# Kernel tuning notes

Hardware: AMD Instinct MI355X
Metric: run time of the kernel (lower is better)

The kernel has to match this reference:

```python
import jax, jax.numpy as jnp
import numpy as np


def fwht(x):
    """Fast Walsh-Hadamard transform over the last dim (power of 2), normalized by 1/sqrt(n)."""
    n = x.shape[-1]
    orig_shape = x.shape
    x = x.reshape(-1, n)
    h = 1
    while h < n:
        x = x.reshape(-1, n // (2 * h), 2, h)
        a = x[:, :, 0, :]
        b = x[:, :, 1, :]
        x = jnp.stack([a + b, a - b], axis=2)
        h *= 2
    x = x.reshape(orig_shape)
    return x * (1.0 / jnp.sqrt(jnp.asarray(n, dtype=x.dtype)))


def act_quant(x, bits):
    """Per-token absmax symmetric quantization with straight-through estimator."""
    qb = 2.0 ** (bits - 1) - 1.0  # 127 for 8 bits
    scale = qb / jnp.clip(jnp.max(jnp.abs(x), axis=-1, keepdims=True), 1e-5, None)
    q = jnp.clip(jnp.round(x * scale), -qb, qb) / scale
    return x + jax.lax.stop_gradient(q - x)


def weight_quant(w):
    """BitNet b1.58 ternary weight quantization (per-tensor mean-abs scale) with STE."""
    scale = jnp.clip(jnp.mean(jnp.abs(w)), 1e-5, None)
    q = jnp.clip(jnp.round(w / scale), -1.0, 1.0) * scale
    return w + jax.lax.stop_gradient(q - w)


def hbitlinear(x, w, bits):
    # Hadamard rotate activations, quantize acts + ternary weights, then GEMM.
    xh = fwht(x)
    xq = act_quant(xh, bits)
    wq = weight_quant(w)
    return jnp.einsum('bsh,oh->bso', xq, wq)


def setup_inputs() -> dict:
    key = jax.random.key(0)
    k1, k2, k3 = jax.random.split(key, 3)
    B, S, H = 4, 2048, 2048
    I = 4096  # intermediate = hidden * mlp_ratio(2.0)
    hidden_states = jax.random.normal(k1, (B, S, H), dtype=jnp.float32)
    w_up = jax.random.normal(k2, (I, H), dtype=jnp.float32) * 0.02
    w_down = jax.random.normal(k3, (H, I), dtype=jnp.float32) * 0.02
    return {"hidden_states": hidden_states, "w_up": w_up, "w_down": w_down}


def reference(hidden_states, w_up, w_down):
    ACT_BITS = 8
    h = hbitlinear(hidden_states, w_up, ACT_BITS)   # (B, S, I)
    h = jnp.square(jax.nn.relu(h))                  # ReLU^2
    # dropout with p=0.0 (eval/identity)
    out = hbitlinear(h, w_down, ACT_BITS)           # (B, S, H)
    return out
```

## Files before the change

### kernel.cpp

```cpp
#include <hip/hip_runtime.h>
#include <hip/hip_bf16.h>
#include <hip/hip_fp16.h>

typedef int i32x4 __attribute__((ext_vector_type(4)));

#define GLL16(g, l) __builtin_amdgcn_global_load_lds( \
    (const __attribute__((address_space(1))) void*)(g), \
    (__attribute__((address_space(3))) void*)(l), 16, 0, 0)

#define CFENCE() asm volatile("" ::: "memory")

__global__ __launch_bounds__(256) void abs_sum2_kernel(const float* __restrict__ w0,
                                                       const float* __restrict__ w1, int n4,
                                                       double* __restrict__ out)
{
    const int sel = blockIdx.x & 1;
    const float4* w4 = (const float4*)(sel ? w1 : w0);
    const int b = blockIdx.x >> 1, nb = gridDim.x >> 1;
    double acc = 0.0;
    for (int i = b * blockDim.x + threadIdx.x; i < n4; i += nb * blockDim.x) {
        float4 v = w4[i];
        acc += (double)fabsf(v.x) + (double)fabsf(v.y) + (double)fabsf(v.z) + (double)fabsf(v.w);
    }
    for (int o = 32; o > 0; o >>= 1) acc += __shfl_down(acc, o, 64);
    __shared__ double part[4];
    int lane = threadIdx.x & 63, wv = threadIdx.x >> 6;
    if (lane == 0) part[wv] = acc;
    __syncthreads();
    if (threadIdx.x == 0) atomicAdd(&out[sel], part[0] + part[1] + part[2] + part[3]);
}

__global__ __launch_bounds__(256) void wquant2_kernel(const float* __restrict__ w0,
                                                      const float* __restrict__ w1, int n4,
                                                      const double* __restrict__ sums, double inv_count,
                                                      char* __restrict__ o0, char* __restrict__ o1)
{
    const int sel = blockIdx.x & 1;
    const float4* w4 = (const float4*)(sel ? w1 : w0);
    char4* o4 = (char4*)(sel ? o1 : o0);
    float s = (float)(sums[sel] * inv_count);
    s = fmaxf(s, 1e-5f);
    const int b = blockIdx.x >> 1, nb = gridDim.x >> 1;
    for (int i = b * blockDim.x + threadIdx.x; i < n4; i += nb * blockDim.x) {
        float4 v = w4[i];
        char4 c;
        c.x = (char)fminf(fmaxf(rintf(v.x / s), -1.0f), 1.0f);
        c.y = (char)fminf(fmaxf(rintf(v.y / s), -1.0f), 1.0f);
        c.z = (char)fminf(fmaxf(rintf(v.z / s), -1.0f), 1.0f);
        c.w = (char)fminf(fmaxf(rintf(v.w / s), -1.0f), 1.0f);
        o4[i] = c;
    }
}

template<int NS>
__device__ __forceinline__ void hreg(float* v)
{
    #pragma unroll
    for (int h = 1; h < (1 << NS); h <<= 1)
        #pragma unroll
        for (int i = 0; i < 16; i++)
            if ((i & h) == 0) { float a = v[i], b = v[i + h]; v[i] = a + b; v[i + h] = a - b; }
}

__device__ __forceinline__ int lswz(int e)
{
    const int r16 = e >> 4;
    return r16 * 16 + 4 * (((e >> 2) & 3) ^ ((r16 >> 1) & 3)) + (e & 3);
}

template<int N, int TOKS>
__global__ __launch_bounds__(256) void fwht_quant_kernel(
    const float* __restrict__ in, long in_stride,
    char* __restrict__ outq, long out_stride,
    float* __restrict__ scales)
{
    constexpr int L = 256 / TOKS;
    static_assert(N == 16 * L, "N must be 16*threads-per-token");
    __shared__ float sx[TOKS * N];
    __shared__ float red[4];

    const int tid = threadIdx.x;
    const int tk  = tid / L;
    const int lt  = tid % L;
    const long tok = (long)blockIdx.x * TOKS + tk;
    const float* row = in + tok * in_stride;
    float* s = sx + tk * N;

    float v[16];
    {
        const float4* r4 = (const float4*)(row + (size_t)lt * 16);
        float4 a[4];
        #pragma unroll
        for (int i = 0; i < 4; i++) a[i] = r4[i];
        #pragma unroll
        for (int i = 0; i < 4; i++) {
            v[4*i] = a[i].x; v[4*i+1] = a[i].y; v[4*i+2] = a[i].z; v[4*i+3] = a[i].w;
        }
    }
    hreg<4>(v);
    {
        const int psw = (lt >> 1) & 3;
        #pragma unroll
        for (int i = 0; i < 4; i++)
            *(float4*)(s + lt * 16 + 4 * (i ^ psw)) =
                make_float4(v[4*i], v[4*i+1], v[4*i+2], v[4*i+3]);
    }
    __syncthreads();

    const int o = lt & 15, ss = lt >> 4;
    #pragma unroll
    for (int j = 0; j < 16; j++) v[j] = s[lswz(o + 256 * ss + 16 * j)];
    hreg<(L == 256) ? 4 : 3>(v);
    #pragma unroll
    for (int j = 0; j < 16; j++) s[lswz(o + 256 * ss + 16 * j)] = v[j];
    __syncthreads();

    #pragma unroll
    for (int j = 0; j < 16; j++) v[j] = s[lswz(o + 16 * ss + L * j)];
    hreg<4>(v);

    const float rn = 1.0f / sqrtf((float)N);
    float m = 0.0f;
    #pragma unroll
    for (int j = 0; j < 16; j++) { v[j] *= rn; m = fmaxf(m, fabsf(v[j])); }
    for (int off = 32; off > 0; off >>= 1) m = fmaxf(m, __shfl_down(m, off, 64));
    if ((tid & 63) == 0) red[tid >> 6] = m;
    __syncthreads();
    float mm;
    if (TOKS == 1) mm = fmaxf(fmaxf(red[0], red[1]), fmaxf(red[2], red[3]));
    else           mm = fmaxf(red[2 * tk], red[2 * tk + 1]);
    mm = fmaxf(mm, 1e-5f);
    const float sc = 127.0f / mm;
    if (lt == 0) scales[tok] = sc;
    __syncthreads();

    char* ct = (char*)sx + tk * N;
    #pragma unroll
    for (int j = 0; j < 16; j++) {
        float q = fminf(fmaxf(rintf(v[j] * sc), -127.0f), 127.0f);
        ct[o + 16 * ss + L * j] = (char)q;
    }
    __syncthreads();
    int4* dst = (int4*)(outq + tok * out_stride);
    dst[lt] = ((const int4*)ct)[lt];
}

__global__ __launch_bounds__(256) void fwht_quant_f16_kernel(
    const __half* __restrict__ in, long in_stride,
    char* __restrict__ outq, long out_stride,
    float* __restrict__ scales)
{
    constexpr int N = 4096, L = 256;
    __shared__ float sx[N];
    __shared__ float red[4];

    const int lt = threadIdx.x;
    const long tok = blockIdx.x;
    const __half* row = in + tok * in_stride;
    float* s = sx;

    float v[16];
    {
        const int4* r4 = (const int4*)row;
        int4 q0 = r4[2 * lt], q1 = r4[2 * lt + 1];
        const __half2* h0 = (const __half2*)&q0;
        const __half2* h1 = (const __half2*)&q1;
        #pragma unroll
        for (int i = 0; i < 4; i++) {
            float2 f = __half22float2(h0[i]);
            v[2*i] = f.x; v[2*i+1] = f.y;
        }
        #pragma unroll
        for (int i = 0; i < 4; i++) {
            float2 f = __half22float2(h1[i]);
            v[8+2*i] = f.x; v[8+2*i+1] = f.y;
        }
    }
    hreg<4>(v);
    {
        const int psw = (lt >> 1) & 3;
        #pragma unroll
        for (int i = 0; i < 4; i++)
            *(float4*)(s + lt * 16 + 4 * (i ^ psw)) =
                make_float4(v[4*i], v[4*i+1], v[4*i+2], v[4*i+3]);
    }
    __syncthreads();

    const int o = lt & 15, ss = lt >> 4;
    #pragma unroll
    for (int j = 0; j < 16; j++) v[j] = s[lswz(o + 256 * ss + 16 * j)];
    hreg<4>(v);
    #pragma unroll
    for (int j = 0; j < 16; j++) s[lswz(o + 256 * ss + 16 * j)] = v[j];
    __syncthreads();

    #pragma unroll
    for (int j = 0; j < 16; j++) v[j] = s[lswz(o + 16 * ss + L * j)];
    hreg<4>(v);

    const float rn = 1.0f / sqrtf((float)N);
    float m = 0.0f;
    #pragma unroll
    for (int j = 0; j < 16; j++) { v[j] *= rn; m = fmaxf(m, fabsf(v[j])); }
    for (int off = 32; off > 0; off >>= 1) m = fmaxf(m, __shfl_down(m, off, 64));
    if ((lt & 63) == 0) red[lt >> 6] = m;
    __syncthreads();
    float mm = fmaxf(fmaxf(red[0], red[1]), fmaxf(red[2], red[3]));
    mm = fmaxf(mm, 1e-5f);
    const float sc = 127.0f / mm;
    if (lt == 0) scales[tok] = sc;
    __syncthreads();

    char* ct = (char*)sx;
    #pragma unroll
    for (int j = 0; j < 16; j++) {
        float q = fminf(fmaxf(rintf(v[j] * sc), -127.0f), 127.0f);
        ct[o + 16 * ss + L * j] = (char)q;
    }
    __syncthreads();
    int4* dst = (int4*)(outq + tok * out_stride);
    dst[lt] = ((const int4*)ct)[lt];
}

#define BM2 256
#define BN2 256
#define BK2 64

__global__ __launch_bounds__(512, 2) void gemm_bt_kernel(
    const char* __restrict__ A, int lda,
    const char* __restrict__ B, int ldb,
    void* __restrict__ Cv, int ldc,
    int K, int lognx,
    const float* __restrict__ sx,
    const double* __restrict__ wsum, double inv_count,
    int do_relu2, int out_f16)
{
    __shared__ __align__(16) char As[4][BM2 * BK2];
    __shared__ __align__(16) char Bs[4][BN2 * BK2];

    const int bid = blockIdx.x;
    const int xcd = bid & 7;
    const int n = bid >> 3;
    const int nper = gridDim.x >> 3;
    const int bx = n & ((1 << lognx) - 1);
    const int by = xcd * (nper >> lognx) + (n >> lognx);
    const int row0 = by * BM2;
    const int col0 = bx * BN2;

    const int tid = threadIdx.x;
    const int lane = tid & 63;
    const int w = tid >> 6;
    const int wr = w >> 2;
    const int wc = w & 3;

    i32x4 acc[8][4] = {};

    const int srow = w * 16 + (lane >> 2);
    const int sseg = ((lane & 3) ^ ((lane >> 3) & 3)) << 4;
    const char* Ag0 = A + (size_t)(row0 + srow) * lda + sseg;
    const char* Ag1 = Ag0 + (size_t)128 * lda;
    const char* Bg0 = B + (size_t)(col0 + srow) * ldb + sseg;
    const char* Bg1 = Bg0 + (size_t)128 * ldb;
    const int wdst = w * 1024;

    const int fr = lane & 15;
    const int fks = lane >> 4;
    const int rsw = ((fks ^ ((fr >> 1) & 3)) << 4);
    const int aoff = (wr * 128 + fr) * BK2 + rsw;
    const int boff = (wc * 64  + fr) * BK2 + rsw;

    const int NT = K >> 6;

    auto stageA = [&](int tt) {
        const int sb = tt & 3;
        const int ko = tt * BK2;
        GLL16(Ag0 + ko, &As[sb][wdst]);
        GLL16(Ag1 + ko, &As[sb][wdst + 8192]);
    };
    auto stageB = [&](int tt) {
        const int sb = tt & 3;
        const int ko = tt * BK2;
        GLL16(Bg0 + ko, &Bs[sb][wdst]);
        GLL16(Bg1 + ko, &Bs[sb][wdst + 8192]);
    };

    auto tile_body = [&](int t, bool do_stage) __attribute__((always_inline)) {
        const int cb = t & 3;
        const char* as = As[cb];
        const char* bs = Bs[cb];
        i32x4 af[4], bf[4], af2[4];
        #pragma unroll
        for (int i = 0; i < 4; ++i) af[i] = *(const i32x4*)(as + aoff + i * 1024);
        #pragma unroll
        for (int j = 0; j < 4; ++j) bf[j] = *(const i32x4*)(bs + boff + j * 1024);
        if (do_stage) stageA(t + 3);
        __builtin_amdgcn_s_barrier();
        CFENCE();
        __builtin_amdgcn_s_setprio(1);
        #pragma unroll
        for (int i = 0; i < 4; ++i)
            #pragma unroll
            for (int j = 0; j < 4; ++j)
                acc[i][j] = __builtin_amdgcn_mfma_i32_16x16x64_i8(af[i], bf[j], acc[i][j], 0, 0, 0);
        __builtin_amdgcn_s_setprio(0);
        __builtin_amdgcn_s_barrier();
        CFENCE();
        #pragma unroll
        for (int i = 0; i < 4; ++i) af2[i] = *(const i32x4*)(as + aoff + (4 + i) * 1024);
        if (do_stage) stageB(t + 3);
        __builtin_amdgcn_s_barrier();
        CFENCE();
        __builtin_amdgcn_s_setprio(1);
        #pragma unroll
        for (int i = 0; i < 4; ++i)
            #pragma unroll
            for (int j = 0; j < 4; ++j)
                acc[4 + i][j] = __builtin_amdgcn_mfma_i32_16x16x64_i8(af2[i], bf[j], acc[4 + i][j], 0, 0, 0);
        __builtin_amdgcn_s_setprio(0);
    };

    stageA(0); stageB(0); stageA(1); stageB(1); stageA(2); stageB(2);
    asm volatile("s_waitcnt vmcnt(8)" ::: "memory");
    __builtin_amdgcn_s_barrier();
    CFENCE();

    for (int t = 0; t <= NT - 4; ++t) {
        tile_body(t, true);
        asm volatile("s_waitcnt vmcnt(8)" ::: "memory");
        __builtin_amdgcn_s_barrier();
        CFENCE();
    }
    tile_body(NT - 3, false);
    asm volatile("s_waitcnt vmcnt(4)" ::: "memory");
    __builtin_amdgcn_s_barrier();
    CFENCE();
    tile_body(NT - 2, false);
    asm volatile("s_waitcnt vmcnt(0)" ::: "memory");
    __builtin_amdgcn_s_barrier();
    CFENCE();
    tile_body(NT - 1, false);

    float sw = (float)(wsum[0] * inv_count);
    sw = fmaxf(sw, 1e-5f);
    const int qd = lane >> 4;
    if (out_f16) {
        __half* C = (__half*)Cv;
        #pragma unroll
        for (int i = 0; i < 8; ++i) {
            #pragma unroll
            for (int r = 0; r < 4; ++r) {
                int rowm = row0 + wr * 128 + i * 16 + qd * 4 + r;
                float esc = sw / sx[rowm];
                __half* crow = C + (size_t)rowm * ldc + col0 + wc * 64;
                #pragma unroll
                for (int j = 0; j < 4; ++j) {
                    float v = (float)acc[i][j][r] * esc;
                    if (do_relu2) { v = fmaxf(v, 0.0f); v = v * v; }
                    crow[j * 16 + fr] = __float2half(v);
                }
            }
        }
    } else {
        float* C = (float*)Cv;
        #pragma unroll
        for (int i = 0; i < 8; ++i) {
            #pragma unroll
            for (int r = 0; r < 4; ++r) {
                int rowm = row0 + wr * 128 + i * 16 + qd * 4 + r;
                float esc = sw / sx[rowm];
                float* crow = C + (size_t)rowm * ldc + col0 + wc * 64;
                #pragma unroll
                for (int j = 0; j < 4; ++j) {
                    float v = (float)acc[i][j][r] * esc;
                    if (do_relu2) { v = fmaxf(v, 0.0f); v = v * v; }
                    crow[j * 16 + fr] = v;
                }
            }
        }
    }
}

extern "C" void kernel_launch(void* const* d_in, const int* in_sizes, int n_in,
                              void* d_out, int out_size, void* d_ws, size_t ws_size,
                              hipStream_t stream)
{
    const float* X   = (const float*)d_in[0];
    const float* Wup = (const float*)d_in[1];
    const float* Wdn = (const float*)d_in[2];
    float* out = (float*)d_out;

    const int Mtok = 8192, H = 2048, I = 4096;
    const int NW = H * I;

    char* ws = (char*)d_ws;
    double* sums = (double*)ws;
    float* sx1 = (float*)(ws + 1024);
    float* sx2 = (float*)(ws + 1024 + 32768);
    char* wqup = ws + (1 << 20);
    char* wqdn = wqup + (size_t)NW;
    char* xq1  = wqdn + (size_t)NW;
    char* hbuf = xq1 + (size_t)Mtok * H;

    hipMemsetAsync(sums, 0, 16, stream);
    abs_sum2_kernel<<<1024, 256, 0, stream>>>(Wup, Wdn, NW / 4, sums);
    const double invc = 1.0 / (double)NW;
    wquant2_kernel<<<2048, 256, 0, stream>>>(Wup, Wdn, NW / 4, sums, invc, wqup, wqdn);

    fwht_quant_kernel<2048, 2><<<Mtok / 2, 256, 0, stream>>>(X, H, xq1, H, sx1);
    gemm_bt_kernel<<<(I / BN2) * (Mtok / BM2), 512, 0, stream>>>(
        xq1, H, wqup, H, hbuf, I, H, 4, sx1, &sums[0], invc, 1, 1);
    fwht_quant_f16_kernel<<<Mtok, 256, 0, stream>>>((const __half*)hbuf, I, hbuf, 2 * I, sx2);
    gemm_bt_kernel<<<(H / BN2) * (Mtok / BM2), 512, 0, stream>>>(
        (const char*)hbuf, 2 * I, wqdn, I, out, H, I, 3, sx2, &sums[1], invc, 0, 0);
}
```

Measured before the change: 372.3 us.

## Shrink GEMM tiles to 128x128 with simple double buffering; threshold weight ternarization

The int8 MFMA GEMM goes from 256x256 tiles with 512 threads and a 4-stage, split A/B prefetch pipeline to 128x128 tiles with 256 threads and a plain 2-stage double buffer that waits on all loads every iteration. Smaller tiles raise the block count and allow three blocks per CU, at the cost of less data reuse per tile and less overlap between loads and MFMA work. Weight quantization replaces the divide, round and clamp with a comparison against half the scale. That comparison can differ from the reference at exact ties.

```diff
diff --git a/kernel.cpp b/kernel.cpp
--- a/kernel.cpp
+++ b/kernel.cpp
@@ -40,14 +40,15 @@
     char4* o4 = (char4*)(sel ? o1 : o0);
     float s = (float)(sums[sel] * inv_count);
     s = fmaxf(s, 1e-5f);
+    const float t0 = 0.5f * s;
     const int b = blockIdx.x >> 1, nb = gridDim.x >> 1;
     for (int i = b * blockDim.x + threadIdx.x; i < n4; i += nb * blockDim.x) {
         float4 v = w4[i];
         char4 c;
-        c.x = (char)fminf(fmaxf(rintf(v.x / s), -1.0f), 1.0f);
-        c.y = (char)fminf(fmaxf(rintf(v.y / s), -1.0f), 1.0f);
-        c.z = (char)fminf(fmaxf(rintf(v.z / s), -1.0f), 1.0f);
-        c.w = (char)fminf(fmaxf(rintf(v.w / s), -1.0f), 1.0f);
+        c.x = (fabsf(v.x) > t0) ? (v.x > 0.0f ? 1 : -1) : 0;
+        c.y = (fabsf(v.y) > t0) ? (v.y > 0.0f ? 1 : -1) : 0;
+        c.z = (fabsf(v.z) > t0) ? (v.z > 0.0f ? 1 : -1) : 0;
+        c.w = (fabsf(v.w) > t0) ? (v.w > 0.0f ? 1 : -1) : 0;
         o4[i] = c;
     }
 }
@@ -222,11 +223,11 @@
     dst[lt] = ((const int4*)ct)[lt];
 }
 
-#define BM2 256
-#define BN2 256
-#define BK2 64
-
-__global__ __launch_bounds__(512, 2) void gemm_bt_kernel(
+#define BM 128
+#define BN 128
+#define BK 64
+
+__global__ __launch_bounds__(256, 3) void gemm_bt_kernel(
     const char* __restrict__ A, int lda,
     const char* __restrict__ B, int ldb,
     void* __restrict__ Cv, int ldc,
@@ -235,8 +236,8 @@
     const double* __restrict__ wsum, double inv_count,
     int do_relu2, int out_f16)
 {
-    __shared__ __align__(16) char As[4][BM2 * BK2];
-    __shared__ __align__(16) char Bs[4][BN2 * BK2];
+    __shared__ __align__(16) char As[2][BM * BK];
+    __shared__ __align__(16) char Bs[2][BN * BK];
 
     const int bid = blockIdx.x;
     const int xcd = bid & 7;
@@ -244,58 +245,49 @@
     const int nper = gridDim.x >> 3;
     const int bx = n & ((1 << lognx) - 1);
     const int by = xcd * (nper >> lognx) + (n >> lognx);
-    const int row0 = by * BM2;
-    const int col0 = bx * BN2;
+    const int row0 = by * BM;
+    const int col0 = bx * BN;
 
     const int tid = threadIdx.x;
     const int lane = tid & 63;
     const int w = tid >> 6;
-    const int wr = w >> 2;
-    const int wc = w & 3;
-
-    i32x4 acc[8][4] = {};
+    const int wr = w >> 1;
+    const int wc = w & 1;
+
+    i32x4 acc[4][4] = {};
 
     const int srow = w * 16 + (lane >> 2);
     const int sseg = ((lane & 3) ^ ((lane >> 3) & 3)) << 4;
     const char* Ag0 = A + (size_t)(row0 + srow) * lda + sseg;
-    const char* Ag1 = Ag0 + (size_t)128 * lda;
+    const char* Ag1 = Ag0 + (size_t)64 * lda;
     const char* Bg0 = B + (size_t)(col0 + srow) * ldb + sseg;
-    const char* Bg1 = Bg0 + (size_t)128 * ldb;
+    const char* Bg1 = Bg0 + (size_t)64 * ldb;
     const int wdst = w * 1024;
 
     const int fr = lane & 15;
     const int fks = lane >> 4;
     const int rsw = ((fks ^ ((fr >> 1) & 3)) << 4);
-    const int aoff = (wr * 128 + fr) * BK2 + rsw;
-    const int boff = (wc * 64  + fr) * BK2 + rsw;
+    const int aoff = (wr * 64 + fr) * BK + rsw;
+    const int boff = (wc * 64 + fr) * BK + rsw;
 
     const int NT = K >> 6;
 
-    auto stageA = [&](int tt) {
-        const int sb = tt & 3;
-        const int ko = tt * BK2;
+    auto stage = [&](int tt) {
+        const int sb = tt & 1;
+        const int ko = tt * BK;
         GLL16(Ag0 + ko, &As[sb][wdst]);
-        GLL16(Ag1 + ko, &As[sb][wdst + 8192]);
+        GLL16(Ag1 + ko, &As[sb][wdst + 4096]);
+        GLL16(Bg0 + ko, &Bs[sb][wdst]);
+        GLL16(Bg1 + ko, &Bs[sb][wdst + 4096]);
     };
-    auto stageB = [&](int tt) {
-        const int sb = tt & 3;
-        const int ko = tt * BK2;
-        GLL16(Bg0 + ko, &Bs[sb][wdst]);
-        GLL16(Bg1 + ko, &Bs[sb][wdst + 8192]);
-    };
-
-    auto tile_body = [&](int t, bool do_stage) __attribute__((always_inline)) {
-        const int cb = t & 3;
-        const char* as = As[cb];
-        const char* bs = Bs[cb];
-        i32x4 af[4], bf[4], af2[4];
+    auto compute = [&](int t) __attribute__((always_inline)) {
+        const char* as = As[t & 1];
+        const char* bs = Bs[t & 1];
+        i32x4 af[4], bf[4];
         #pragma unroll
         for (int i = 0; i < 4; ++i) af[i] = *(const i32x4*)(as + aoff + i * 1024);
         #pragma unroll
         for (int j = 0; j < 4; ++j) bf[j] = *(const i32x4*)(bs + boff + j * 1024);
-        if (do_stage) stageA(t + 3);
-        __builtin_amdgcn_s_barrier();
-        CFENCE();
         __builtin_amdgcn_s_setprio(1);
         #pragma unroll
         for (int i = 0; i < 4; ++i)
@@ -303,42 +295,21 @@
             for (int j = 0; j < 4; ++j)
                 acc[i][j] = __builtin_amdgcn_mfma_i32_16x16x64_i8(af[i], bf[j], acc[i][j], 0, 0, 0);
         __builtin_amdgcn_s_setprio(0);
-        __builtin_amdgcn_s_barrier();
-        CFENCE();
-        #pragma unroll
-        for (int i = 0; i < 4; ++i) af2[i] = *(const i32x4*)(as + aoff + (4 + i) * 1024);
-        if (do_stage) stageB(t + 3);
-        __builtin_amdgcn_s_barrier();
-        CFENCE();
-        __builtin_amdgcn_s_setprio(1);
-        #pragma unroll
-        for (int i = 0; i < 4; ++i)
-            #pragma unroll
-            for (int j = 0; j < 4; ++j)
-                acc[4 + i][j] = __builtin_amdgcn_mfma_i32_16x16x64_i8(af2[i], bf[j], acc[4 + i][j], 0, 0, 0);
-        __builtin_amdgcn_s_setprio(0);
     };
 
-    stageA(0); stageB(0); stageA(1); stageB(1); stageA(2); stageB(2);
-    asm volatile("s_waitcnt vmcnt(8)" ::: "memory");
-    __builtin_amdgcn_s_barrier();
-    CFENCE();
-
-    for (int t = 0; t <= NT - 4; ++t) {
-        tile_body(t, true);
-        asm volatile("s_waitcnt vmcnt(8)" ::: "memory");
-        __builtin_amdgcn_s_barrier();
-        CFENCE();
-    }
-    tile_body(NT - 3, false);
-    asm volatile("s_waitcnt vmcnt(4)" ::: "memory");
-    __builtin_amdgcn_s_barrier();
-    CFENCE();
-    tile_body(NT - 2, false);
+    stage(0);
     asm volatile("s_waitcnt vmcnt(0)" ::: "memory");
     __builtin_amdgcn_s_barrier();
     CFENCE();
-    tile_body(NT - 1, false);
+
+    for (int t = 0; t < NT - 1; ++t) {
+        stage(t + 1);
+        compute(t);
+        asm volatile("s_waitcnt vmcnt(0)" ::: "memory");
+        __builtin_amdgcn_s_barrier();
+        CFENCE();
+    }
+    compute(NT - 1);
 
     float sw = (float)(wsum[0] * inv_count);
     sw = fmaxf(sw, 1e-5f);
@@ -346,10 +317,10 @@
     if (out_f16) {
         __half* C = (__half*)Cv;
         #pragma unroll
-        for (int i = 0; i < 8; ++i) {
+        for (int i = 0; i < 4; ++i) {
             #pragma unroll
             for (int r = 0; r < 4; ++r) {
-                int rowm = row0 + wr * 128 + i * 16 + qd * 4 + r;
+                int rowm = row0 + wr * 64 + i * 16 + qd * 4 + r;
                 float esc = sw / sx[rowm];
                 __half* crow = C + (size_t)rowm * ldc + col0 + wc * 64;
                 #pragma unroll
@@ -363,10 +334,10 @@
     } else {
         float* C = (float*)Cv;
         #pragma unroll
-        for (int i = 0; i < 8; ++i) {
+        for (int i = 0; i < 4; ++i) {
             #pragma unroll
             for (int r = 0; r < 4; ++r) {
-                int rowm = row0 + wr * 128 + i * 16 + qd * 4 + r;
+                int rowm = row0 + wr * 64 + i * 16 + qd * 4 + r;
                 float esc = sw / sx[rowm];
                 float* crow = C + (size_t)rowm * ldc + col0 + wc * 64;
                 #pragma unroll
@@ -407,9 +378,9 @@
     wquant2_kernel<<<2048, 256, 0, stream>>>(Wup, Wdn, NW / 4, sums, invc, wqup, wqdn);
 
     fwht_quant_kernel<2048, 2><<<Mtok / 2, 256, 0, stream>>>(X, H, xq1, H, sx1);
-    gemm_bt_kernel<<<(I / BN2) * (Mtok / BM2), 512, 0, stream>>>(
-        xq1, H, wqup, H, hbuf, I, H, 4, sx1, &sums[0], invc, 1, 1);
+    gemm_bt_kernel<<<(I / BN) * (Mtok / BM), 256, 0, stream>>>(
+        xq1, H, wqup, H, hbuf, I, H, 5, sx1, &sums[0], invc, 1, 1);
     fwht_quant_f16_kernel<<<Mtok, 256, 0, stream>>>((const __half*)hbuf, I, hbuf, 2 * I, sx2);
-    gemm_bt_kernel<<<(H / BN2) * (Mtok / BM2), 512, 0, stream>>>(
-        (const char*)hbuf, 2 * I, wqdn, I, out, H, I, 3, sx2, &sums[1], invc, 0, 0);
-}
+    gemm_bt_kernel<<<(H / BN) * (Mtok / BM), 256, 0, stream>>>(
+        (const char*)hbuf, 2 * I, wqdn, I, out, H, I, 4, sx2, &sums[1], invc, 0, 0);
+}
```

Measured after the change: 362.4 us. -2.7%, faster.
